# Performance work log

Hardware: AMD Instinct MI355X
Metric: run time of the kernel (lower is better)

Reference implementation:

```python
import jax, jax.numpy as jnp
import numpy as np

NUM_HOP = 3
VOCAB = 32000
D = 512          # embed_dim
MEM = 60         # memory_size (> story_size -> T_A slice branch)
BS = 64
STORY = 50
SENT = 32        # max_sent_size
QLEN = 16


def positional_encoding(J, d):
    # pe[i-1, k-1] = 1 - i/J - (k/d) * (1 - 2*i/J), i in 1..J, k in 1..d
    i = jnp.arange(1, J + 1, dtype=jnp.float32)[:, None]
    k = jnp.arange(1, d + 1, dtype=jnp.float32)[None, :]
    return 1.0 - i / J - (k / d) * (1.0 - 2.0 * i / J)


def setup_inputs() -> dict:
    key = jax.random.key(0)
    kA, kT, kC, kQ = jax.random.split(key, 4)
    # stacked embedding tables A[0..num_hop], each (VOCAB, D), N(0, 0.1)
    A = jax.random.normal(kA, (NUM_HOP + 1, VOCAB, D), dtype=jnp.float32) * 0.1
    T_A = jax.random.normal(kT, (1, MEM, D), dtype=jnp.float32) * 0.1
    context = jax.random.randint(kC, (BS, STORY, SENT), 0, VOCAB)
    query = jax.random.randint(kQ, (BS, QLEN), 0, VOCAB)
    return {"context": context, "query": query, "A": A, "T_A": T_A}


def reference(context, query, A, T_A):
    # padding_idx=0: row 0 of every table is zero
    A = A.at[:, 0, :].set(0.0)
    pe = positional_encoding(SENT, D)              # (SENT, D)

    # query encoding: u = B(query).sum(axis=1), B = A[0]; dropout is identity at eval
    u = A[0][query].sum(axis=1)                    # (BS, D)

    for h in range(NUM_HOP):
        # memory embedding with positional encoding, summed over words
        m = (A[h][context] * pe).sum(axis=2)       # (BS, STORY, D)
        # temporal encoding: memory_size > story_size branch
        m = m + T_A[:, :STORY, :]
        # output embedding (no positional encoding applied in original)
        c = A[h + 1][context].sum(axis=2)          # (BS, STORY, D)
        p = jax.nn.softmax(jnp.einsum('bsd,bd->bs', m, u), axis=1)
        u = u + jnp.einsum('bs,bsd->bd', p, c)

    # W = A[-1].weight.T -> logits = u @ W
    logits = u @ A[NUM_HOP].T                      # (BS, VOCAB)
    return jax.nn.softmax(logits, axis=-1)
```

## Files before the change

kernel.cpp:

```cpp
#include <hip/hip_runtime.h>
#include <math.h>

#define NUM_HOP 3
#define VOCAB   32000
#define DIM     512
#define MEM     60
#define BS      64
#define STORY   50
#define SENT    32
#define QLEN    16

typedef short v8s __attribute__((ext_vector_type(8)));
typedef float v4f __attribute__((ext_vector_type(4)));

static __device__ __forceinline__ ushort f2bf(float x) {
    union { float f; unsigned u; } v; v.f = x;
    unsigned r = (v.u + 0x7FFFu + ((v.u >> 16) & 1u)) >> 16;
    return (ushort)r;
}

__global__ void k_pass(const float* __restrict__ table,
                       const int*   __restrict__ ctx,
                       const int*   __restrict__ query,
                       float*       __restrict__ mw,
                       float*       __restrict__ c,
                       float*       __restrict__ u,
                       int write_mw, int write_c, int do_query) {
    const int blk = blockIdx.x;
    const int d   = threadIdx.x * 4;
    if (do_query && blk >= BS * STORY) {
        const int b = blk - BS * STORY;
        const int* q = query + b * QLEN;
        float4 acc = make_float4(0.f, 0.f, 0.f, 0.f);
        for (int t = 0; t < QLEN; ++t) {
            const int idx = q[t];
            if (idx != 0) {
                const float4 a = *(const float4*)(table + (size_t)idx * DIM + d);
                acc.x += a.x; acc.y += a.y; acc.z += a.z; acc.w += a.w;
            }
        }
        *(float4*)(u + (size_t)b * DIM + d) = acc;
        return;
    }
    const int* cw = ctx + blk * SENT;
    float4 m  = make_float4(0.f, 0.f, 0.f, 0.f);
    float4 cc = make_float4(0.f, 0.f, 0.f, 0.f);
    const float invD = 1.0f / (float)DIM;
    #pragma unroll 8
    for (int w = 0; w < SENT; ++w) {
        const int idx = cw[w];
        if (idx == 0) continue;
        const float4 a = *(const float4*)(table + (size_t)idx * DIM + d);
        const float aw = 1.0f - (float)(w + 1) * (1.0f / (float)SENT);
        const float bw = 1.0f - (float)(2 * (w + 1)) * (1.0f / (float)SENT);
        const float p0 = aw - bw * (float)(d + 1) * invD;
        const float p1 = aw - bw * (float)(d + 2) * invD;
        const float p2 = aw - bw * (float)(d + 3) * invD;
        const float p3 = aw - bw * (float)(d + 4) * invD;
        m.x = fmaf(a.x, p0, m.x);
        m.y = fmaf(a.y, p1, m.y);
        m.z = fmaf(a.z, p2, m.z);
        m.w = fmaf(a.w, p3, m.w);
        cc.x += a.x; cc.y += a.y; cc.z += a.z; cc.w += a.w;
    }
    if (write_mw) *(float4*)(mw + (size_t)blk * DIM + d) = m;
    if (write_c)  *(float4*)(c  + (size_t)blk * DIM + d) = cc;
}

__global__ __launch_bounds__(256) void k_hop(const float* __restrict__ mw,
                                             const float* __restrict__ c,
                                             const float* __restrict__ T_A,
                                             float*       __restrict__ u,
                                             ushort*      __restrict__ ubf) {
    const int b    = blockIdx.x;
    const int tid  = threadIdx.x;
    const int wave = tid >> 6;
    const int lane = tid & 63;
    __shared__ float sw[64];

    const float* ub = u + (size_t)b * DIM;
    const float4 u0 = *(const float4*)(ub + lane * 8);
    const float4 u1 = *(const float4*)(ub + lane * 8 + 4);

    for (int s = wave; s < STORY; s += 4) {
        const float* mrow = mw  + ((size_t)b * STORY + s) * DIM + lane * 8;
        const float* trow = T_A + (size_t)s * DIM + lane * 8;
        const float4 m0 = *(const float4*)(mrow);
        const float4 m1 = *(const float4*)(mrow + 4);
        const float4 t0 = *(const float4*)(trow);
        const float4 t1 = *(const float4*)(trow + 4);
        float p = (m0.x + t0.x) * u0.x + (m0.y + t0.y) * u0.y +
                  (m0.z + t0.z) * u0.z + (m0.w + t0.w) * u0.w +
                  (m1.x + t1.x) * u1.x + (m1.y + t1.y) * u1.y +
                  (m1.z + t1.z) * u1.z + (m1.w + t1.w) * u1.w;
        for (int off = 32; off; off >>= 1) p += __shfl_down(p, off);
        if (lane == 0) sw[s] = p;
    }
    __syncthreads();

    if (tid < 64) {
        const float v = (tid < STORY) ? sw[tid] : -1e30f;
        float mx = v;
        for (int off = 32; off; off >>= 1) mx = fmaxf(mx, __shfl_down(mx, off));
        mx = __shfl(mx, 0);
        const float e = (tid < STORY) ? __expf(v - mx) : 0.f;
        float sm = e;
        for (int off = 32; off; off >>= 1) sm += __shfl_down(sm, off);
        sm = __shfl(sm, 0);
        if (tid < STORY) sw[tid] = e / sm;
    }
    __syncthreads();

    const int d = tid * 2;
    float2 acc = *(const float2*)(ub + d);
    const float* crow = c + (size_t)b * STORY * DIM + d;
    #pragma unroll 5
    for (int s = 0; s < STORY; ++s) {
        const float  w  = sw[s];
        const float2 cc = *(const float2*)(crow + (size_t)s * DIM);
        acc.x = fmaf(w, cc.x, acc.x);
        acc.y = fmaf(w, cc.y, acc.y);
    }
    *(float2*)(u + (size_t)b * DIM + d) = acc;
    if (ubf) {
        ubf[b * DIM + d]     = f2bf(acc.x);
        ubf[b * DIM + d + 1] = f2bf(acc.y);
    }
}

__global__ __launch_bounds__(256) void k_logits(const float*  __restrict__ A3,
                                                const ushort* __restrict__ ubf,
                                                float*        __restrict__ out) {
    __shared__ ushort Abf[64 * 128];
    __shared__ ushort Ubf[64 * 128];
    const int tid  = threadIdx.x;
    const int lane = tid & 63;
    const int wave = tid >> 6;
    const int i16  = lane & 15;
    const int quad = lane >> 4;
    const int row0 = blockIdx.x * 64;

    v4f acc[4];
    #pragma unroll
    for (int nt = 0; nt < 4; ++nt) acc[nt] = (v4f){0.f, 0.f, 0.f, 0.f};

    for (int ko = 0; ko < 4; ++ko) {
        __syncthreads();
        #pragma unroll
        for (int it = 0; it < 4; ++it) {
            const int i = it * 256 + tid;
            const int r = i >> 4, g = i & 15;
            const float* src = A3 + ((size_t)(row0 + r)) * DIM + ko * 128 + g * 8;
            const float4 f0 = *(const float4*)(src);
            const float4 f1 = *(const float4*)(src + 4);
            union { ushort h[8]; uint4 q; } pk;
            pk.h[0] = f2bf(f0.x); pk.h[1] = f2bf(f0.y);
            pk.h[2] = f2bf(f0.z); pk.h[3] = f2bf(f0.w);
            pk.h[4] = f2bf(f1.x); pk.h[5] = f2bf(f1.y);
            pk.h[6] = f2bf(f1.z); pk.h[7] = f2bf(f1.w);
            *(uint4*)(&Abf[r * 128 + ((g ^ (r & 7)) * 8)]) = pk.q;
        }
        #pragma unroll
        for (int it = 0; it < 4; ++it) {
            const int i = it * 256 + tid;
            const int n = i >> 4, g = i & 15;
            const uint4 v = *(const uint4*)(ubf + (size_t)n * DIM + ko * 128 + g * 8);
            *(uint4*)(&Ubf[n * 128 + ((g ^ (n & 7)) * 8)]) = v;
        }
        __syncthreads();

        const int arow = wave * 16 + i16;
        #pragma unroll
        for (int ki = 0; ki < 4; ++ki) {
            const int ga = ki * 4 + quad;
            const v8s a = *(const v8s*)(&Abf[arow * 128 + ((ga ^ (arow & 7)) * 8)]);
            #pragma unroll
            for (int nt = 0; nt < 4; ++nt) {
                const int n = nt * 16 + i16;
                const v8s bb = *(const v8s*)(&Ubf[n * 128 + ((ga ^ (n & 7)) * 8)]);
                acc[nt] = __builtin_amdgcn_mfma_f32_16x16x32_bf16(a, bb, acc[nt], 0, 0, 0);
            }
        }
    }

    const int vbase = row0 + wave * 16 + quad * 4;
    #pragma unroll
    for (int nt = 0; nt < 4; ++nt) {
        const int bcol = nt * 16 + i16;
        #pragma unroll
        for (int r = 0; r < 4; ++r)
            out[(size_t)bcol * VOCAB + vbase + r] = acc[nt][r];
    }
}

__global__ void k_vsm(float* __restrict__ out) {
    const int b = blockIdx.x;
    float* row = out + (size_t)b * VOCAB;
    const int tid = threadIdx.x;
    __shared__ float red[256];
    float mx = -1e30f;
    for (int v = tid; v < VOCAB; v += 256) mx = fmaxf(mx, row[v]);
    red[tid] = mx; __syncthreads();
    for (int off = 128; off; off >>= 1) {
        if (tid < off) red[tid] = fmaxf(red[tid], red[tid + off]);
        __syncthreads();
    }
    mx = red[0]; __syncthreads();
    float sum = 0.f;
    for (int v = tid; v < VOCAB; v += 256) sum += __expf(row[v] - mx);
    red[tid] = sum; __syncthreads();
    for (int off = 128; off; off >>= 1) {
        if (tid < off) red[tid] += red[tid + off];
        __syncthreads();
    }
    const float inv = 1.0f / red[0];
    for (int v = tid; v < VOCAB; v += 256) row[v] = __expf(row[v] - mx) * inv;
}

extern "C" void kernel_launch(void* const* d_in, const int* in_sizes, int n_in,
                              void* d_out, int out_size, void* d_ws, size_t ws_size,
                              hipStream_t stream) {
    const int*   ctx   = (const int*)d_in[0];
    const int*   query = (const int*)d_in[1];
    const float* A     = (const float*)d_in[2];
    const float* T_A   = (const float*)d_in[3];
    float* out = (float*)d_out;

    float*  u   = (float*)d_ws;
    ushort* ubf = (ushort*)(u + (size_t)BS * DIM);
    float*  buf = (float*)(ubf + (size_t)BS * DIM);
    const size_t SZ = (size_t)BS * STORY * DIM;
    float* mw0 = buf;
    float* mw1 = mw0 + SZ;
    float* mw2 = mw1 + SZ;
    float* c0  = mw2 + SZ;
    float* c1  = c0 + SZ;
    float* c2  = c1 + SZ;

    const size_t TBL = (size_t)VOCAB * DIM;

    k_pass<<<BS * STORY + BS, 128, 0, stream>>>(A,           ctx, query, mw0, nullptr, u, 1, 0, 1);
    k_pass<<<BS * STORY,      128, 0, stream>>>(A + TBL,     ctx, query, mw1, c0,      u, 1, 1, 0);
    k_pass<<<BS * STORY,      128, 0, stream>>>(A + 2 * TBL, ctx, query, mw2, c1,      u, 1, 1, 0);
    k_pass<<<BS * STORY,      128, 0, stream>>>(A + 3 * TBL, ctx, query, nullptr, c2,  u, 0, 1, 0);

    k_hop<<<BS, 256, 0, stream>>>(mw0, c0, T_A, u, nullptr);
    k_hop<<<BS, 256, 0, stream>>>(mw1, c1, T_A, u, nullptr);
    k_hop<<<BS, 256, 0, stream>>>(mw2, c2, T_A, u, ubf);

    k_logits<<<VOCAB / 64, 256, 0, stream>>>(A + 3 * TBL, ubf, out);
    k_vsm   <<<BS, 256, 0, stream>>>(out);
}
```

Before: 528.3 us.

## Fuse gather passes and hop kernels into single launches, register-cache vocab softmax

The four per-table gather kernels are merged into one launch that covers every table plus the query sum. The three hop kernels become one 512-thread kernel that keeps u in shared memory across hops and splits the weighted c-sum across eight waves. The vocabulary softmax now uses 1024 threads and holds each row in registers, so it reads the row once instead of three times and uses wave shuffles for the reductions. The aim is to cut launch count and global memory traffic, at the cost of higher register pressure in the softmax kernel.

After: 455.6 us. 13.8% less time.

```diff
diff --git a/kernel.cpp b/kernel.cpp
--- a/kernel.cpp
+++ b/kernel.cpp
@@ -10,6 +10,9 @@
 #define SENT    32
 #define QLEN    16
 
+#define SZ      ((size_t)BS * STORY * DIM)
+#define TBL     ((size_t)VOCAB * DIM)
+
 typedef short v8s __attribute__((ext_vector_type(8)));
 typedef float v4f __attribute__((ext_vector_type(4)));
 
@@ -19,30 +22,33 @@
     return (ushort)r;
 }
 
-__global__ void k_pass(const float* __restrict__ table,
-                       const int*   __restrict__ ctx,
-                       const int*   __restrict__ query,
-                       float*       __restrict__ mw,
-                       float*       __restrict__ c,
-                       float*       __restrict__ u,
-                       int write_mw, int write_c, int do_query) {
-    const int blk = blockIdx.x;
-    const int d   = threadIdx.x * 4;
-    if (do_query && blk >= BS * STORY) {
-        const int b = blk - BS * STORY;
+__global__ __launch_bounds__(128) void k_gather(const float* __restrict__ A,
+                                                const int*   __restrict__ ctx,
+                                                const int*   __restrict__ query,
+                                                float*       __restrict__ mw,
+                                                float*       __restrict__ c,
+                                                float*       __restrict__ u) {
+    const unsigned blk = blockIdx.x;
+    const int d = threadIdx.x * 4;
+    if (blk >= 4u * BS * STORY) {
+        const int b = blk - 4u * BS * STORY;
         const int* q = query + b * QLEN;
         float4 acc = make_float4(0.f, 0.f, 0.f, 0.f);
         for (int t = 0; t < QLEN; ++t) {
             const int idx = q[t];
             if (idx != 0) {
-                const float4 a = *(const float4*)(table + (size_t)idx * DIM + d);
+                const float4 a = *(const float4*)(A + (size_t)idx * DIM + d);
                 acc.x += a.x; acc.y += a.y; acc.z += a.z; acc.w += a.w;
             }
         }
         *(float4*)(u + (size_t)b * DIM + d) = acc;
         return;
     }
-    const int* cw = ctx + blk * SENT;
+    const unsigned pass = blk / (BS * STORY);
+    const unsigned bs   = blk - pass * (BS * STORY);
+    const float* table = A + (size_t)pass * TBL;
+    const int*   cw    = ctx + bs * SENT;
+
     float4 m  = make_float4(0.f, 0.f, 0.f, 0.f);
     float4 cc = make_float4(0.f, 0.f, 0.f, 0.f);
     const float invD = 1.0f / (float)DIM;
@@ -53,79 +59,91 @@
         const float4 a = *(const float4*)(table + (size_t)idx * DIM + d);
         const float aw = 1.0f - (float)(w + 1) * (1.0f / (float)SENT);
         const float bw = 1.0f - (float)(2 * (w + 1)) * (1.0f / (float)SENT);
-        const float p0 = aw - bw * (float)(d + 1) * invD;
-        const float p1 = aw - bw * (float)(d + 2) * invD;
-        const float p2 = aw - bw * (float)(d + 3) * invD;
-        const float p3 = aw - bw * (float)(d + 4) * invD;
-        m.x = fmaf(a.x, p0, m.x);
-        m.y = fmaf(a.y, p1, m.y);
-        m.z = fmaf(a.z, p2, m.z);
-        m.w = fmaf(a.w, p3, m.w);
+        m.x = fmaf(a.x, aw - bw * (float)(d + 1) * invD, m.x);
+        m.y = fmaf(a.y, aw - bw * (float)(d + 2) * invD, m.y);
+        m.z = fmaf(a.z, aw - bw * (float)(d + 3) * invD, m.z);
+        m.w = fmaf(a.w, aw - bw * (float)(d + 4) * invD, m.w);
         cc.x += a.x; cc.y += a.y; cc.z += a.z; cc.w += a.w;
     }
-    if (write_mw) *(float4*)(mw + (size_t)blk * DIM + d) = m;
-    if (write_c)  *(float4*)(c  + (size_t)blk * DIM + d) = cc;
-}
-
-__global__ __launch_bounds__(256) void k_hop(const float* __restrict__ mw,
-                                             const float* __restrict__ c,
-                                             const float* __restrict__ T_A,
-                                             float*       __restrict__ u,
-                                             ushort*      __restrict__ ubf) {
+    if (pass < 3) *(float4*)(mw + (size_t)pass * SZ + (size_t)bs * DIM + d) = m;
+    if (pass > 0) *(float4*)(c + (size_t)(pass - 1) * SZ + (size_t)bs * DIM + d) = cc;
+}
+
+__global__ __launch_bounds__(512) void k_hops(const float* __restrict__ mw,
+                                              const float* __restrict__ c,
+                                              const float* __restrict__ T_A,
+                                              const float* __restrict__ u_g,
+                                              ushort*      __restrict__ ubf) {
     const int b    = blockIdx.x;
     const int tid  = threadIdx.x;
     const int wave = tid >> 6;
     const int lane = tid & 63;
+    __shared__ float su[DIM];
     __shared__ float sw[64];
-
-    const float* ub = u + (size_t)b * DIM;
-    const float4 u0 = *(const float4*)(ub + lane * 8);
-    const float4 u1 = *(const float4*)(ub + lane * 8 + 4);
-
-    for (int s = wave; s < STORY; s += 4) {
-        const float* mrow = mw  + ((size_t)b * STORY + s) * DIM + lane * 8;
-        const float* trow = T_A + (size_t)s * DIM + lane * 8;
-        const float4 m0 = *(const float4*)(mrow);
-        const float4 m1 = *(const float4*)(mrow + 4);
-        const float4 t0 = *(const float4*)(trow);
-        const float4 t1 = *(const float4*)(trow + 4);
-        float p = (m0.x + t0.x) * u0.x + (m0.y + t0.y) * u0.y +
-                  (m0.z + t0.z) * u0.z + (m0.w + t0.w) * u0.w +
-                  (m1.x + t1.x) * u1.x + (m1.y + t1.y) * u1.y +
-                  (m1.z + t1.z) * u1.z + (m1.w + t1.w) * u1.w;
-        for (int off = 32; off; off >>= 1) p += __shfl_down(p, off);
-        if (lane == 0) sw[s] = p;
-    }
-    __syncthreads();
-
-    if (tid < 64) {
-        const float v = (tid < STORY) ? sw[tid] : -1e30f;
-        float mx = v;
-        for (int off = 32; off; off >>= 1) mx = fmaxf(mx, __shfl_down(mx, off));
-        mx = __shfl(mx, 0);
-        const float e = (tid < STORY) ? __expf(v - mx) : 0.f;
-        float sm = e;
-        for (int off = 32; off; off >>= 1) sm += __shfl_down(sm, off);
-        sm = __shfl(sm, 0);
-        if (tid < STORY) sw[tid] = e / sm;
-    }
-    __syncthreads();
-
-    const int d = tid * 2;
-    float2 acc = *(const float2*)(ub + d);
-    const float* crow = c + (size_t)b * STORY * DIM + d;
-    #pragma unroll 5
-    for (int s = 0; s < STORY; ++s) {
-        const float  w  = sw[s];
-        const float2 cc = *(const float2*)(crow + (size_t)s * DIM);
-        acc.x = fmaf(w, cc.x, acc.x);
-        acc.y = fmaf(w, cc.y, acc.y);
-    }
-    *(float2*)(u + (size_t)b * DIM + d) = acc;
-    if (ubf) {
-        ubf[b * DIM + d]     = f2bf(acc.x);
-        ubf[b * DIM + d + 1] = f2bf(acc.y);
-    }
+    __shared__ float up[8][DIM];
+
+    su[tid] = u_g[(size_t)b * DIM + tid];
+    __syncthreads();
+
+    for (int h = 0; h < NUM_HOP; ++h) {
+        const float* mwh = mw + (size_t)h * SZ + (size_t)b * STORY * DIM;
+        const float* ch  = c  + (size_t)h * SZ + (size_t)b * STORY * DIM;
+
+        const float4 u0 = *(const float4*)(&su[lane * 8]);
+        const float4 u1 = *(const float4*)(&su[lane * 8 + 4]);
+        for (int s = wave; s < STORY; s += 8) {
+            const float* mrow = mwh + (size_t)s * DIM + lane * 8;
+            const float* trow = T_A + (size_t)s * DIM + lane * 8;
+            const float4 m0 = *(const float4*)(mrow);
+            const float4 m1 = *(const float4*)(mrow + 4);
+            const float4 t0 = *(const float4*)(trow);
+            const float4 t1 = *(const float4*)(trow + 4);
+            float p = (m0.x + t0.x) * u0.x + (m0.y + t0.y) * u0.y +
+                      (m0.z + t0.z) * u0.z + (m0.w + t0.w) * u0.w +
+                      (m1.x + t1.x) * u1.x + (m1.y + t1.y) * u1.y +
+                      (m1.z + t1.z) * u1.z + (m1.w + t1.w) * u1.w;
+            for (int off = 32; off; off >>= 1) p += __shfl_down(p, off);
+            if (lane == 0) sw[s] = p;
+        }
+        __syncthreads();
+
+        if (tid < 64) {
+            const float v = (tid < STORY) ? sw[tid] : -1e30f;
+            float mx = v;
+            for (int off = 32; off; off >>= 1) mx = fmaxf(mx, __shfl_down(mx, off));
+            mx = __shfl(mx, 0);
+            const float e = (tid < STORY) ? __expf(v - mx) : 0.f;
+            float sm = e;
+            for (int off = 32; off; off >>= 1) sm += __shfl_down(sm, off);
+            sm = __shfl(sm, 0);
+            if (tid < STORY) sw[tid] = e / sm;
+        }
+        __syncthreads();
+
+        float4 a0 = make_float4(0.f, 0.f, 0.f, 0.f);
+        float4 a1 = make_float4(0.f, 0.f, 0.f, 0.f);
+        for (int s = wave; s < STORY; s += 8) {
+            const float  w    = sw[s];
+            const float* crow = ch + (size_t)s * DIM + lane * 8;
+            const float4 c0 = *(const float4*)(crow);
+            const float4 c1 = *(const float4*)(crow + 4);
+            a0.x = fmaf(w, c0.x, a0.x); a0.y = fmaf(w, c0.y, a0.y);
+            a0.z = fmaf(w, c0.z, a0.z); a0.w = fmaf(w, c0.w, a0.w);
+            a1.x = fmaf(w, c1.x, a1.x); a1.y = fmaf(w, c1.y, a1.y);
+            a1.z = fmaf(w, c1.z, a1.z); a1.w = fmaf(w, c1.w, a1.w);
+        }
+        *(float4*)(&up[wave][lane * 8])     = a0;
+        *(float4*)(&up[wave][lane * 8 + 4]) = a1;
+        __syncthreads();
+
+        float add = 0.f;
+        #pragma unroll
+        for (int w = 0; w < 8; ++w) add += up[w][tid];
+        su[tid] += add;
+        __syncthreads();
+    }
+
+    ubf[(size_t)b * DIM + tid] = f2bf(su[tid]);
 }
 
 __global__ __launch_bounds__(256) void k_logits(const float*  __restrict__ A3,
@@ -193,28 +211,52 @@
     }
 }
 
-__global__ void k_vsm(float* __restrict__ out) {
-    const int b = blockIdx.x;
+__global__ __launch_bounds__(1024) void k_vsm(float* __restrict__ out) {
+    const int b   = blockIdx.x;
+    const int tid = threadIdx.x;
     float* row = out + (size_t)b * VOCAB;
-    const int tid = threadIdx.x;
-    __shared__ float red[256];
+    __shared__ float red[16];
+    __shared__ float bc;
+
+    float x[32];
+    #pragma unroll
+    for (int k = 0; k < 31; ++k) x[k] = row[tid + k * 1024];
+    const bool extra = (tid < VOCAB - 31 * 1024);
+    x[31] = extra ? row[tid + 31 * 1024] : -1e30f;
+
     float mx = -1e30f;
-    for (int v = tid; v < VOCAB; v += 256) mx = fmaxf(mx, row[v]);
-    red[tid] = mx; __syncthreads();
-    for (int off = 128; off; off >>= 1) {
-        if (tid < off) red[tid] = fmaxf(red[tid], red[tid + off]);
-        __syncthreads();
-    }
-    mx = red[0]; __syncthreads();
+    #pragma unroll
+    for (int k = 0; k < 32; ++k) mx = fmaxf(mx, x[k]);
+    for (int off = 32; off; off >>= 1) mx = fmaxf(mx, __shfl_down(mx, off));
+    if ((tid & 63) == 0) red[tid >> 6] = mx;
+    __syncthreads();
+    if (tid < 64) {
+        float v = (tid < 16) ? red[tid] : -1e30f;
+        for (int off = 8; off; off >>= 1) v = fmaxf(v, __shfl_down(v, off));
+        if (tid == 0) bc = v;
+    }
+    __syncthreads();
+    mx = bc;
+    __syncthreads();
+
     float sum = 0.f;
-    for (int v = tid; v < VOCAB; v += 256) sum += __expf(row[v] - mx);
-    red[tid] = sum; __syncthreads();
-    for (int off = 128; off; off >>= 1) {
-        if (tid < off) red[tid] += red[tid + off];
-        __syncthreads();
-    }
-    const float inv = 1.0f / red[0];
-    for (int v = tid; v < VOCAB; v += 256) row[v] = __expf(row[v] - mx) * inv;
+    #pragma unroll
+    for (int k = 0; k < 32; ++k) { x[k] = __expf(x[k] - mx); sum += x[k]; }
+    if (!extra) sum -= x[31];
+    for (int off = 32; off; off >>= 1) sum += __shfl_down(sum, off);
+    if ((tid & 63) == 0) red[tid >> 6] = sum;
+    __syncthreads();
+    if (tid < 64) {
+        float v = (tid < 16) ? red[tid] : 0.f;
+        for (int off = 8; off; off >>= 1) v += __shfl_down(v, off);
+        if (tid == 0) bc = v;
+    }
+    __syncthreads();
+    const float inv = 1.0f / bc;
+
+    #pragma unroll
+    for (int k = 0; k < 31; ++k) row[tid + k * 1024] = x[k] * inv;
+    if (extra) row[tid + 31 * 1024] = x[31] * inv;
 }
 
 extern "C" void kernel_launch(void* const* d_in, const int* in_sizes, int n_in,
@@ -228,26 +270,11 @@
 
     float*  u   = (float*)d_ws;
     ushort* ubf = (ushort*)(u + (size_t)BS * DIM);
-    float*  buf = (float*)(ubf + (size_t)BS * DIM);
-    const size_t SZ = (size_t)BS * STORY * DIM;
-    float* mw0 = buf;
-    float* mw1 = mw0 + SZ;
-    float* mw2 = mw1 + SZ;
-    float* c0  = mw2 + SZ;
-    float* c1  = c0 + SZ;
-    float* c2  = c1 + SZ;
-
-    const size_t TBL = (size_t)VOCAB * DIM;
-
-    k_pass<<<BS * STORY + BS, 128, 0, stream>>>(A,           ctx, query, mw0, nullptr, u, 1, 0, 1);
-    k_pass<<<BS * STORY,      128, 0, stream>>>(A + TBL,     ctx, query, mw1, c0,      u, 1, 1, 0);
-    k_pass<<<BS * STORY,      128, 0, stream>>>(A + 2 * TBL, ctx, query, mw2, c1,      u, 1, 1, 0);
-    k_pass<<<BS * STORY,      128, 0, stream>>>(A + 3 * TBL, ctx, query, nullptr, c2,  u, 0, 1, 0);
-
-    k_hop<<<BS, 256, 0, stream>>>(mw0, c0, T_A, u, nullptr);
-    k_hop<<<BS, 256, 0, stream>>>(mw1, c1, T_A, u, nullptr);
-    k_hop<<<BS, 256, 0, stream>>>(mw2, c2, T_A, u, ubf);
-
+    float*  mw  = (float*)(ubf + (size_t)BS * DIM);
+    float*  c   = mw + 3 * SZ;
+
+    k_gather<<<4 * BS * STORY + BS, 128, 0, stream>>>(A, ctx, query, mw, c, u);
+    k_hops  <<<BS, 512, 0, stream>>>(mw, c, T_A, u, ubf);
     k_logits<<<VOCAB / 64, 256, 0, stream>>>(A + 3 * TBL, ubf, out);
-    k_vsm   <<<BS, 256, 0, stream>>>(out);
-}
+    k_vsm   <<<BS, 1024, 0, stream>>>(out);
+}
```
